# Optimization experiments

Hardware: AMD Instinct MI355X
Metric: run time of the kernel (lower is better)

Reference implementation:

```python
import jax, jax.numpy as jnp
import numpy as np

B, S, D = 2, 2048, 2048
H, HD, M = 16, 128, 8192
EPS = 1e-6

def _rmsnorm(x, scale):
    var = jnp.mean(jnp.square(x), axis=-1, keepdims=True)
    return x * jax.lax.rsqrt(var + EPS) * scale

def setup_inputs() -> dict:
    key = jax.random.key(0)
    ks = jax.random.split(key, 8)
    def init(k, shape, fan_in):
        return (jax.random.normal(k, shape, dtype=jnp.float32) / np.sqrt(fan_in)).astype(jnp.float32)
    return {
        "x": jax.random.normal(ks[0], (B, S, D), dtype=jnp.float32),
        "w_qkv": init(ks[1], (D, 3 * H * HD), D),
        "w_o": init(ks[2], (H * HD, D), H * HD),
        "w_gate": init(ks[3], (D, M), D),
        "w_up": init(ks[4], (D, M), D),
        "w_down": init(ks[5], (M, D), M),
        "rms1_scale": jnp.ones((D,), dtype=jnp.float32),
        "rms2_scale": jnp.ones((D,), dtype=jnp.float32),
    }

def reference(x, w_qkv, w_o, w_gate, w_up, w_down, rms1_scale, rms2_scale):
    batch, seq_len, embed_dim = x.shape
    # --- attention sub-block ---
    residual = x
    h = _rmsnorm(x, rms1_scale)
    qkv = h @ w_qkv  # [B,S,3*H*HD]
    qkv = qkv.reshape(batch, seq_len, 3, H, HD)
    q, k, v = qkv[:, :, 0], qkv[:, :, 1], qkv[:, :, 2]
    scale = 1.0 / jnp.sqrt(jnp.float32(HD))
    scores = jnp.einsum('bqhd,bkhd->bhqk', q, k) * scale  # materialized [B,H,S,S]
    mask = jnp.tril(jnp.ones((seq_len, seq_len), dtype=jnp.bool_))[None, None]
    scores = jnp.where(mask, scores, jnp.finfo(scores.dtype).min)
    weights = jax.nn.softmax(scores.astype(jnp.float32), axis=-1).astype(scores.dtype)
    attn_out = jnp.einsum('bhqk,bkhd->bqhd', weights, v)
    attn_out = attn_out.reshape(batch, seq_len, -1) @ w_o
    x = residual + attn_out
    # --- SwiGLU MLP sub-block ---
    residual = x
    h = _rmsnorm(x, rms2_scale)
    gate = h @ w_gate
    up = h @ w_up
    mlp = (jax.nn.silu(gate) * up) @ w_down
    return residual + mlp
```

## Files before the change

### kernel.cpp

```cpp
#include <hip/hip_runtime.h>
#include <cstdint>

#define DEV __device__ __forceinline__

typedef __attribute__((ext_vector_type(8))) short bf16x8;
typedef __attribute__((ext_vector_type(4))) float f32x4;

DEV unsigned short f2bf(float f) {
    unsigned u = __float_as_uint(f);
    return (unsigned short)((u + 0x8000u) >> 16);
}
DEV float bf2f(unsigned short h) { return __uint_as_float(((unsigned)h) << 16); }

DEV void gld_lds16(const void* g, void* l) {
    __builtin_amdgcn_global_load_lds(
        (const __attribute__((address_space(1))) unsigned int*)g,
        (__attribute__((address_space(3))) unsigned int*)l,
        16, 0, 0);
}

DEV bf16x8 scale_frag(bf16x8 v, float s) {
    bf16x8 r;
#pragma unroll
    for (int i = 0; i < 8; ++i)
        r[i] = (short)f2bf(bf2f((unsigned short)v[i]) * s);
    return r;
}

__global__ __launch_bounds__(256) void rmsnorm_kernel(const float* __restrict__ x,
                                                      const float* __restrict__ scale,
                                                      unsigned short* __restrict__ h) {
    const long row = blockIdx.x;
    const int t = threadIdx.x;
    const float4* xr = (const float4*)(x + row * 2048);
    float4 a = xr[t];
    float4 b = xr[t + 256];
    float ss = a.x*a.x + a.y*a.y + a.z*a.z + a.w*a.w
             + b.x*b.x + b.y*b.y + b.z*b.z + b.w*b.w;
#pragma unroll
    for (int off = 32; off >= 1; off >>= 1) ss += __shfl_xor(ss, off);
    __shared__ float red[4];
    if ((t & 63) == 0) red[t >> 6] = ss;
    __syncthreads();
    const float rr = rsqrtf((red[0] + red[1] + red[2] + red[3]) * (1.0f / 2048.0f) + 1e-6f);
    const float4* sc = (const float4*)scale;
    float4 s0 = sc[t], s1 = sc[t + 256];
    ushort4 o0 = make_ushort4(f2bf(a.x*rr*s0.x), f2bf(a.y*rr*s0.y), f2bf(a.z*rr*s0.z), f2bf(a.w*rr*s0.w));
    ushort4 o1 = make_ushort4(f2bf(b.x*rr*s1.x), f2bf(b.y*rr*s1.y), f2bf(b.z*rr*s1.z), f2bf(b.w*rr*s1.w));
    ushort4* hr = (ushort4*)(h + row * 2048);
    hr[t] = o0;
    hr[t + 256] = o1;
}

__global__ __launch_bounds__(256) void wcvt_kernel(const float* __restrict__ in,
                                                   unsigned short* __restrict__ out,
                                                   int K, int N) {
    __shared__ float tile[64][65];
    const int k0 = blockIdx.y * 64, n0 = blockIdx.x * 64;
    const int t = threadIdx.x;
    const int tr = t >> 4;
    const int tc = (t & 15) * 4;
#pragma unroll
    for (int p = 0; p < 4; ++p) {
        const int k = p * 16 + tr;
        float4 v = *(const float4*)&in[(long)(k0 + k) * N + n0 + tc];
        tile[k][tc] = v.x; tile[k][tc + 1] = v.y; tile[k][tc + 2] = v.z; tile[k][tc + 3] = v.w;
    }
    __syncthreads();
#pragma unroll
    for (int p = 0; p < 4; ++p) {
        const int n = p * 16 + tr;
        ushort4 o = make_ushort4(f2bf(tile[tc][n]), f2bf(tile[tc + 1][n]),
                                 f2bf(tile[tc + 2][n]), f2bf(tile[tc + 3][n]));
        *(ushort4*)&out[(long)(n0 + n) * K + k0 + tc] = o;
    }
}

template <int EPI>
__global__ __launch_bounds__(256) void gemm_kernel(const unsigned short* __restrict__ A,
                                                   const unsigned short* __restrict__ BT,
                                                   void* __restrict__ Cv,
                                                   const float* __restrict__ res,
                                                   int M, int N, int K) {
    __shared__ short A_lds[128 * 64];
    __shared__ short B_lds[128 * 64];

    const int t = threadIdx.x;
    const int wave = t >> 6, lane = t & 63;
    const int quad = lane >> 4, l16 = lane & 15;
    const int wm = wave >> 1, wn = wave & 1;
    const long m0 = (long)blockIdx.y * 128;
    const long n0 = (long)blockIdx.x * 128;

    f32x4 acc[4][4] = {};

    const int srow = lane >> 3;
    const int scol = (((lane & 7) ^ srow) << 3);

    for (int k0 = 0; k0 < K; k0 += 64) {
#pragma unroll
        for (int j = 0; j < 4; ++j) {
            gld_lds16(A + (m0 + wave * 32 + j * 8 + srow) * (long)K + k0 + scol,
                      &A_lds[(wave * 32 + j * 8) * 64]);
            gld_lds16(BT + (n0 + wave * 32 + j * 8 + srow) * (long)K + k0 + scol,
                      &B_lds[(wave * 32 + j * 8) * 64]);
        }
        __syncthreads();
#pragma unroll
        for (int ks = 0; ks < 2; ++ks) {
            bf16x8 af[4], bf[4];
#pragma unroll
            for (int i = 0; i < 4; ++i) {
                const int cs = ((ks * 4 + quad) ^ (l16 & 7)) << 3;
                af[i] = *(const bf16x8*)&A_lds[(wm * 64 + i * 16 + l16) * 64 + cs];
                bf[i] = *(const bf16x8*)&B_lds[(wn * 64 + i * 16 + l16) * 64 + cs];
            }
#pragma unroll
            for (int mt = 0; mt < 4; ++mt)
#pragma unroll
                for (int nt = 0; nt < 4; ++nt)
                    acc[mt][nt] = __builtin_amdgcn_mfma_f32_16x16x32_bf16(af[mt], bf[nt], acc[mt][nt], 0, 0, 0);
        }
        __syncthreads();
    }

#pragma unroll
    for (int mt = 0; mt < 4; ++mt) {
        const long rbase = m0 + wm * 64 + mt * 16 + quad * 4;
#pragma unroll
        for (int nt = 0; nt < 4; ++nt) {
            const long col = n0 + wn * 64 + nt * 16 + l16;
#pragma unroll
            for (int r = 0; r < 4; ++r) {
                const long idx = (rbase + r) * (long)N + col;
                const float v = acc[mt][nt][r];
                if (EPI == 0) {
                    ((unsigned short*)Cv)[idx] = f2bf(v);
                } else if (EPI == 1) {
                    ((float*)Cv)[idx] = res[idx] + v;
                } else {
                    unsigned short* C = (unsigned short*)Cv;
                    const float g = bf2f(C[idx]);
                    const float sg = g / (1.0f + __expf(-g));
                    C[idx] = f2bf(sg * v);
                }
            }
        }
    }
}

__global__ __launch_bounds__(256, 4) void attn_kernel(const unsigned short* __restrict__ qkv,
                                                      unsigned short* __restrict__ outp) {
    __shared__ short K_lds[64 * 128];
    __shared__ short V_lds[128 * 64];
    __shared__ short P_lds[4 * 16 * 64];

    const int b = blockIdx.z;
    const int qt = (b == 0) ? blockIdx.x : (31 - blockIdx.x);
    const int hh = blockIdx.y;
    const int t = threadIdx.x;
    const int wave = t >> 6, lane = t & 63, quad = lane >> 4, l16 = lane & 15;
    const long rb = (long)b * 2048;
    const int q0w = qt * 64 + wave * 16;
    const int qmax = q0w + 15;
    const float scale = 0.08838834764831845f;

    bf16x8 qf[4];
#pragma unroll
    for (int ks = 0; ks < 4; ++ks)
        qf[ks] = scale_frag(
            *(const bf16x8*)&qkv[(rb + q0w + l16) * 6144 + hh * 128 + ks * 32 + quad * 8],
            scale);

    f32x4 acc[8] = {};
    float l_lane = 0.f;

    const int ktiles = qt + 1;
    const int nc = t & 31, kq0 = (t >> 5) << 1;

    for (int kt = 0; kt < ktiles; ++kt) {
        const int k0 = kt * 64;
#pragma unroll
        for (int j = 0; j < 4; ++j) {
            const int r8 = (j * 4 + quad) & 7;
            const int csrc = ((l16 & 8) | ((l16 & 7) ^ r8)) << 3;
            gld_lds16(&qkv[(rb + k0 + wave * 16 + j * 4 + quad) * 6144 + 2048 + hh * 128 + csrc],
                      &K_lds[(wave * 16 + j * 4) * 128]);
        }
#pragma unroll
        for (int g2 = 0; g2 < 2; ++g2) {
            const int kq = kq0 + g2;
            const unsigned short* Vp = &qkv[(rb + k0 + kq * 4) * 6144 + 4096 + hh * 128 + nc * 4];
            ushort4 v0 = *(const ushort4*)Vp;
            ushort4 v1 = *(const ushort4*)(Vp + 6144);
            ushort4 v2 = *(const ushort4*)(Vp + 12288);
            ushort4 v3 = *(const ushort4*)(Vp + 18432);
            const int cs = (((kq >> 1) ^ (nc & 7)) << 3) + ((kq & 1) << 2);
            const int db = (nc * 4) * 64 + cs;
            *(ushort4*)&V_lds[db      ] = make_ushort4(v0.x, v1.x, v2.x, v3.x);
            *(ushort4*)&V_lds[db + 64 ] = make_ushort4(v0.y, v1.y, v2.y, v3.y);
            *(ushort4*)&V_lds[db + 128] = make_ushort4(v0.z, v1.z, v2.z, v3.z);
            *(ushort4*)&V_lds[db + 192] = make_ushort4(v0.w, v1.w, v2.w, v3.w);
        }
        __syncthreads();

        if (k0 <= qmax) {
            f32x4 sa[4] = {};
#pragma unroll
            for (int ks = 0; ks < 4; ++ks) {
#pragma unroll
                for (int mt = 0; mt < 4; ++mt) {
                    const int cl = ks * 4 + quad;
                    const int cphys = (cl & 8) | ((cl & 7) ^ (l16 & 7));
                    bf16x8 kf = *(const bf16x8*)&K_lds[(mt * 16 + l16) * 128 + (cphys << 3)];
                    sa[mt] = __builtin_amdgcn_mfma_f32_16x16x32_bf16(kf, qf[ks], sa[mt], 0, 0, 0);
                }
            }
            const bool domask = (k0 + 63 > q0w);
            const int qpos = q0w + l16;
#pragma unroll
            for (int mt = 0; mt < 4; ++mt) {
                const int kb = k0 + mt * 16 + quad * 4;
                ushort4 pk;
#pragma unroll
                for (int r = 0; r < 4; ++r) {
                    float s = (domask && (kb + r > qpos)) ? -1e30f : sa[mt][r];
                    float p = __expf(s);
                    l_lane += p;
                    ((unsigned short*)&pk)[r] = f2bf(p);
                }
                const int chks = (mt * 2 + (quad >> 1)) ^ (l16 & 7);
                *(ushort4*)&P_lds[wave * 1024 + l16 * 64 + chks * 8 + (quad & 1) * 4] = pk;
            }
            __asm__ __volatile__("s_waitcnt lgkmcnt(0)" ::: "memory");
#pragma unroll
            for (int kp = 0; kp < 2; ++kp) {
                bf16x8 pf = *(const bf16x8*)&P_lds[wave * 1024 + l16 * 64 +
                                                   (((kp * 4 + quad) ^ (l16 & 7)) << 3)];
#pragma unroll
                for (int dt = 0; dt < 8; ++dt) {
                    bf16x8 vf = *(const bf16x8*)&V_lds[(dt * 16 + l16) * 64 +
                                                       (((kp * 4 + quad) ^ ((dt * 4 + (l16 >> 2)) & 7)) << 3)];
                    acc[dt] = __builtin_amdgcn_mfma_f32_16x16x32_bf16(vf, pf, acc[dt], 0, 0, 0);
                }
            }
        }
        __syncthreads();
    }

    l_lane += __shfl_xor(l_lane, 16);
    l_lane += __shfl_xor(l_lane, 32);
    const float inv = 1.0f / l_lane;

    const long obase = (rb + q0w + l16) * 2048 + hh * 128;
#pragma unroll
    for (int dt = 0; dt < 8; ++dt) {
        ushort4 o;
#pragma unroll
        for (int r = 0; r < 4; ++r) ((unsigned short*)&o)[r] = f2bf(acc[dt][r] * inv);
        *(ushort4*)&outp[obase + dt * 16 + quad * 4] = o;
    }
}

extern "C" void kernel_launch(void* const* d_in, const int* in_sizes, int n_in,
                              void* d_out, int out_size, void* d_ws, size_t ws_size,
                              hipStream_t stream) {
    const float* x      = (const float*)d_in[0];
    const float* w_qkv  = (const float*)d_in[1];
    const float* w_o    = (const float*)d_in[2];
    const float* w_gate = (const float*)d_in[3];
    const float* w_up   = (const float*)d_in[4];
    const float* w_down = (const float*)d_in[5];
    const float* rms1   = (const float*)d_in[6];
    const float* rms2   = (const float*)d_in[7];
    float* out = (float*)d_out;

    char* ws = (char*)d_ws;
    unsigned short* wT      = (unsigned short*)(ws);
    unsigned short* h       = (unsigned short*)(ws + 33554432);
    unsigned short* qkv     = (unsigned short*)(ws + 50331648);
    unsigned short* attnout = (unsigned short*)(ws + 100663296);
    unsigned short* act     = qkv;

    rmsnorm_kernel<<<4096, 256, 0, stream>>>(x, rms1, h);

    wcvt_kernel<<<dim3(96, 32), 256, 0, stream>>>(w_qkv, wT, 2048, 6144);
    gemm_kernel<0><<<dim3(48, 32), 256, 0, stream>>>(h, wT, (void*)qkv, nullptr, 4096, 6144, 2048);

    attn_kernel<<<dim3(32, 16, 2), 256, 0, stream>>>(qkv, attnout);

    wcvt_kernel<<<dim3(32, 32), 256, 0, stream>>>(w_o, wT, 2048, 2048);
    gemm_kernel<1><<<dim3(16, 32), 256, 0, stream>>>(attnout, wT, (void*)out, x, 4096, 2048, 2048);

    rmsnorm_kernel<<<4096, 256, 0, stream>>>(out, rms2, h);

    wcvt_kernel<<<dim3(128, 32), 256, 0, stream>>>(w_gate, wT, 2048, 8192);
    gemm_kernel<0><<<dim3(64, 32), 256, 0, stream>>>(h, wT, (void*)act, nullptr, 4096, 8192, 2048);

    wcvt_kernel<<<dim3(128, 32), 256, 0, stream>>>(w_up, wT, 2048, 8192);
    gemm_kernel<2><<<dim3(64, 32), 256, 0, stream>>>(h, wT, (void*)act, nullptr, 4096, 8192, 2048);

    wcvt_kernel<<<dim3(32, 128), 256, 0, stream>>>(w_down, wT, 8192, 2048);
    gemm_kernel<1><<<dim3(16, 32), 256, 0, stream>>>(act, wT, (void*)out, out, 4096, 2048, 8192);
}
```

Measured before the change: 1.032 ms.

## Rewrite GEMM with larger 256xBN tiles, 8 waves, and double-buffered LDS prefetch

```diff
diff --git a/kernel.cpp b/kernel.cpp
--- a/kernel.cpp
+++ b/kernel.cpp
@@ -76,57 +76,145 @@
     }
 }
 
-template <int EPI>
-__global__ __launch_bounds__(256) void gemm_kernel(const unsigned short* __restrict__ A,
-                                                   const unsigned short* __restrict__ BT,
-                                                   void* __restrict__ Cv,
-                                                   const float* __restrict__ res,
-                                                   int M, int N, int K) {
-    __shared__ short A_lds[128 * 64];
-    __shared__ short B_lds[128 * 64];
+template <int BN, int EPI>
+__global__ __launch_bounds__(512, 2) void gemm_kernel(const unsigned short* __restrict__ A,
+                                                      const unsigned short* __restrict__ BT,
+                                                      void* __restrict__ Cv,
+                                                      const float* __restrict__ res,
+                                                      int M, int N, int K) {
+    constexpr int WN = BN / 64;
+    constexpr int WM = 8 / WN;
+    constexpr int RW = 256 / WM;
+    constexpr int MT = RW / 16;
+    constexpr int MH = MT / 2;
+
+    __shared__ short A_lds[2][256 * 64];
+    __shared__ short B_lds[2][BN * 64];
 
     const int t = threadIdx.x;
     const int wave = t >> 6, lane = t & 63;
     const int quad = lane >> 4, l16 = lane & 15;
-    const int wm = wave >> 1, wn = wave & 1;
-    const long m0 = (long)blockIdx.y * 128;
-    const long n0 = (long)blockIdx.x * 128;
-
-    f32x4 acc[4][4] = {};
+    const int wm = wave / WN, wn = wave % WN;
+    const long m0 = (long)blockIdx.y * 256;
+    const long n0 = (long)blockIdx.x * BN;
 
     const int srow = lane >> 3;
-    const int scol = (((lane & 7) ^ srow) << 3);
-
-    for (int k0 = 0; k0 < K; k0 += 64) {
-#pragma unroll
-        for (int j = 0; j < 4; ++j) {
-            gld_lds16(A + (m0 + wave * 32 + j * 8 + srow) * (long)K + k0 + scol,
-                      &A_lds[(wave * 32 + j * 8) * 64]);
-            gld_lds16(BT + (n0 + wave * 32 + j * 8 + srow) * (long)K + k0 + scol,
-                      &B_lds[(wave * 32 + j * 8) * 64]);
-        }
-        __syncthreads();
-#pragma unroll
-        for (int ks = 0; ks < 2; ++ks) {
-            bf16x8 af[4], bf[4];
-#pragma unroll
-            for (int i = 0; i < 4; ++i) {
-                const int cs = ((ks * 4 + quad) ^ (l16 & 7)) << 3;
-                af[i] = *(const bf16x8*)&A_lds[(wm * 64 + i * 16 + l16) * 64 + cs];
-                bf[i] = *(const bf16x8*)&B_lds[(wn * 64 + i * 16 + l16) * 64 + cs];
-            }
-#pragma unroll
-            for (int mt = 0; mt < 4; ++mt)
-#pragma unroll
-                for (int nt = 0; nt < 4; ++nt)
-                    acc[mt][nt] = __builtin_amdgcn_mfma_f32_16x16x32_bf16(af[mt], bf[nt], acc[mt][nt], 0, 0, 0);
-        }
-        __syncthreads();
-    }
-
-#pragma unroll
-    for (int mt = 0; mt < 4; ++mt) {
-        const long rbase = m0 + wm * 64 + mt * 16 + quad * 4;
+    const int scol = ((lane & 7) ^ srow) << 3;
+    const int nkt = K >> 6;
+
+    int aoff[MT][2], boff[4][2];
+#pragma unroll
+    for (int mt = 0; mt < MT; ++mt)
+#pragma unroll
+        for (int ks = 0; ks < 2; ++ks)
+            aoff[mt][ks] = (wm * RW + mt * 16 + l16) * 64 + ((((ks << 2) + quad) ^ (l16 & 7)) << 3);
+#pragma unroll
+    for (int nt = 0; nt < 4; ++nt)
+#pragma unroll
+        for (int ks = 0; ks < 2; ++ks)
+            boff[nt][ks] = (wn * 64 + nt * 16 + l16) * 64 + ((((ks << 2) + quad) ^ (l16 & 7)) << 3);
+
+    const unsigned short* Ag = A + (m0 + wave * 32 + srow) * (long)K + scol;
+    const unsigned short* Bg = BT + (n0 + wave * (8 * WN) + srow) * (long)K + scol;
+
+    auto stage = [&](int kt, int buf) {
+        const long kk = (long)kt << 6;
+#pragma unroll
+        for (int j = 0; j < 4; ++j)
+            gld_lds16(Ag + (long)j * 8 * K + kk, &A_lds[buf][(wave * 32 + j * 8) * 64]);
+#pragma unroll
+        for (int j = 0; j < WN; ++j)
+            gld_lds16(Bg + (long)j * 8 * K + kk, &B_lds[buf][(wave * 8 * WN + j * 8) * 64]);
+    };
+
+    f32x4 acc[MT][4] = {};
+
+    stage(0, 0);
+    stage(1, 1);
+    if constexpr (WN == 4) asm volatile("s_waitcnt vmcnt(8)" ::: "memory");
+    else                   asm volatile("s_waitcnt vmcnt(6)" ::: "memory");
+    __builtin_amdgcn_s_barrier();
+
+    int c = 0;
+    for (int kt = 0; kt < nkt; ++kt) {
+        const short* Ab = A_lds[c];
+        const short* Bb = B_lds[c];
+        bf16x8 bfr[4][2], afr[MH][2];
+#pragma unroll
+        for (int nt = 0; nt < 4; ++nt)
+#pragma unroll
+            for (int ks = 0; ks < 2; ++ks)
+                bfr[nt][ks] = *(const bf16x8*)&Bb[boff[nt][ks]];
+#pragma unroll
+        for (int mt = 0; mt < MH; ++mt)
+#pragma unroll
+            for (int ks = 0; ks < 2; ++ks)
+                afr[mt][ks] = *(const bf16x8*)&Ab[aoff[mt][ks]];
+
+        __builtin_amdgcn_s_setprio(1);
+#pragma unroll
+        for (int ks = 0; ks < 2; ++ks)
+#pragma unroll
+            for (int mt = 0; mt < MH; ++mt)
+#pragma unroll
+                for (int nt = 0; nt < 2; ++nt)
+                    acc[mt][nt] = __builtin_amdgcn_mfma_f32_16x16x32_bf16(afr[mt][ks], bfr[nt][ks], acc[mt][nt], 0, 0, 0);
+        __builtin_amdgcn_s_setprio(0);
+        __builtin_amdgcn_s_barrier();
+
+        __builtin_amdgcn_s_setprio(1);
+#pragma unroll
+        for (int ks = 0; ks < 2; ++ks)
+#pragma unroll
+            for (int mt = 0; mt < MH; ++mt)
+#pragma unroll
+                for (int nt = 2; nt < 4; ++nt)
+                    acc[mt][nt] = __builtin_amdgcn_mfma_f32_16x16x32_bf16(afr[mt][ks], bfr[nt][ks], acc[mt][nt], 0, 0, 0);
+        __builtin_amdgcn_s_setprio(0);
+        __builtin_amdgcn_s_barrier();
+
+#pragma unroll
+        for (int mt = 0; mt < MH; ++mt)
+#pragma unroll
+            for (int ks = 0; ks < 2; ++ks)
+                afr[mt][ks] = *(const bf16x8*)&Ab[aoff[MH + mt][ks]];
+        __builtin_amdgcn_s_setprio(1);
+#pragma unroll
+        for (int ks = 0; ks < 2; ++ks)
+#pragma unroll
+            for (int mt = 0; mt < MH; ++mt)
+#pragma unroll
+                for (int nt = 2; nt < 4; ++nt)
+                    acc[MH + mt][nt] = __builtin_amdgcn_mfma_f32_16x16x32_bf16(afr[mt][ks], bfr[nt][ks], acc[MH + mt][nt], 0, 0, 0);
+        __builtin_amdgcn_s_setprio(0);
+        __builtin_amdgcn_s_barrier();
+
+        __builtin_amdgcn_s_setprio(1);
+#pragma unroll
+        for (int ks = 0; ks < 2; ++ks)
+#pragma unroll
+            for (int mt = 0; mt < MH; ++mt)
+#pragma unroll
+                for (int nt = 0; nt < 2; ++nt)
+                    acc[MH + mt][nt] = __builtin_amdgcn_mfma_f32_16x16x32_bf16(afr[mt][ks], bfr[nt][ks], acc[MH + mt][nt], 0, 0, 0);
+        __builtin_amdgcn_s_setprio(0);
+
+        asm volatile("s_waitcnt lgkmcnt(0)" ::: "memory");
+        __builtin_amdgcn_s_barrier();
+        if (kt + 2 < nkt) {
+            stage(kt + 2, c);
+            if constexpr (WN == 4) asm volatile("s_waitcnt vmcnt(8)" ::: "memory");
+            else                   asm volatile("s_waitcnt vmcnt(6)" ::: "memory");
+        } else {
+            asm volatile("s_waitcnt vmcnt(0)" ::: "memory");
+        }
+        __builtin_amdgcn_s_barrier();
+        c ^= 1;
+    }
+
+#pragma unroll
+    for (int mt = 0; mt < MT; ++mt) {
+        const long rbase = m0 + wm * RW + mt * 16 + quad * 4;
 #pragma unroll
         for (int nt = 0; nt < 4; ++nt) {
             const long col = n0 + wn * 64 + nt * 16 + l16;
@@ -134,9 +222,9 @@
             for (int r = 0; r < 4; ++r) {
                 const long idx = (rbase + r) * (long)N + col;
                 const float v = acc[mt][nt][r];
-                if (EPI == 0) {
+                if constexpr (EPI == 0) {
                     ((unsigned short*)Cv)[idx] = f2bf(v);
-                } else if (EPI == 1) {
+                } else if constexpr (EPI == 1) {
                     ((float*)Cv)[idx] = res[idx] + v;
                 } else {
                     unsigned short* C = (unsigned short*)Cv;
@@ -285,21 +373,21 @@
     rmsnorm_kernel<<<4096, 256, 0, stream>>>(x, rms1, h);
 
     wcvt_kernel<<<dim3(96, 32), 256, 0, stream>>>(w_qkv, wT, 2048, 6144);
-    gemm_kernel<0><<<dim3(48, 32), 256, 0, stream>>>(h, wT, (void*)qkv, nullptr, 4096, 6144, 2048);
+    gemm_kernel<128, 0><<<dim3(48, 16), 512, 0, stream>>>(h, wT, (void*)qkv, nullptr, 4096, 6144, 2048);
 
     attn_kernel<<<dim3(32, 16, 2), 256, 0, stream>>>(qkv, attnout);
 
     wcvt_kernel<<<dim3(32, 32), 256, 0, stream>>>(w_o, wT, 2048, 2048);
-    gemm_kernel<1><<<dim3(16, 32), 256, 0, stream>>>(attnout, wT, (void*)out, x, 4096, 2048, 2048);
+    gemm_kernel<128, 1><<<dim3(16, 16), 512, 0, stream>>>(attnout, wT, (void*)out, x, 4096, 2048, 2048);
 
     rmsnorm_kernel<<<4096, 256, 0, stream>>>(out, rms2, h);
 
     wcvt_kernel<<<dim3(128, 32), 256, 0, stream>>>(w_gate, wT, 2048, 8192);
-    gemm_kernel<0><<<dim3(64, 32), 256, 0, stream>>>(h, wT, (void*)act, nullptr, 4096, 8192, 2048);
+    gemm_kernel<256, 0><<<dim3(32, 16), 512, 0, stream>>>(h, wT, (void*)act, nullptr, 4096, 8192, 2048);
 
     wcvt_kernel<<<dim3(128, 32), 256, 0, stream>>>(w_up, wT, 2048, 8192);
-    gemm_kernel<2><<<dim3(64, 32), 256, 0, stream>>>(h, wT, (void*)act, nullptr, 4096, 8192, 2048);
+    gemm_kernel<256, 2><<<dim3(32, 16), 512, 0, stream>>>(h, wT, (void*)act, nullptr, 4096, 8192, 2048);
 
     wcvt_kernel<<<dim3(32, 128), 256, 0, stream>>>(w_down, wT, 8192, 2048);
-    gemm_kernel<1><<<dim3(16, 32), 256, 0, stream>>>(act, wT, (void*)out, out, 4096, 2048, 8192);
-}
+    gemm_kernel<128, 1><<<dim3(16, 16), 512, 0, stream>>>(act, wT, (void*)out, out, 4096, 2048, 8192);
+}
```

Result: slower. 1.096 ms (+6.1%).

## Rewrite GEMM as 8-wave double-buffered pipelined kernel with larger tiles

Applied to the files above, without the earlier changes.

```diff
diff --git a/kernel.cpp b/kernel.cpp
--- a/kernel.cpp
+++ b/kernel.cpp
@@ -76,67 +76,146 @@
     }
 }
 
-template <int EPI>
-__global__ __launch_bounds__(256) void gemm_kernel(const unsigned short* __restrict__ A,
-                                                   const unsigned short* __restrict__ BT,
-                                                   void* __restrict__ Cv,
-                                                   const float* __restrict__ res,
-                                                   int M, int N, int K) {
-    __shared__ short A_lds[128 * 64];
-    __shared__ short B_lds[128 * 64];
+#define BARRIER() asm volatile("s_barrier" ::: "memory")
+#define PRE_MM()  { BARRIER(); asm volatile("s_waitcnt lgkmcnt(0)" ::: "memory"); \
+                    __builtin_amdgcn_sched_barrier(0); }
+
+#define RD_A(Ab, Mh_)                                                             \
+  { _Pragma("unroll") for (int mt = 0; mt < MTQ; ++mt)                            \
+      _Pragma("unroll") for (int ks = 0; ks < 2; ++ks)                            \
+        ar[mt][ks] = *(const bf16x8*)&(Ab)[((Mh_) * (BM / 2) + qm * (BM / 4)      \
+            + mt * 16 + l16) * 64 + ((((ks << 2) + quad) ^ axor) << 3)]; }
+
+#define RD_B(Bb, Nh_)                                                             \
+  { _Pragma("unroll") for (int nt = 0; nt < 2; ++nt)                              \
+      _Pragma("unroll") for (int ks = 0; ks < 2; ++ks)                            \
+        br[nt][ks] = *(const bf16x8*)&(Bb)[((Nh_) * 128 + qn * 32 + nt * 16       \
+            + l16) * 64 + ((((ks << 2) + quad) ^ axor) << 3)]; }
+
+#define MM(Mh_, Nh_)                                                              \
+  { __builtin_amdgcn_s_setprio(1);                                               \
+    _Pragma("unroll") for (int ks = 0; ks < 2; ++ks)                              \
+      _Pragma("unroll") for (int mt = 0; mt < MTQ; ++mt)                          \
+        _Pragma("unroll") for (int nt = 0; nt < 2; ++nt)                          \
+          acc[Mh_][mt][Nh_][nt] = __builtin_amdgcn_mfma_f32_16x16x32_bf16(        \
+              ar[mt][ks], br[nt][ks], acc[Mh_][mt][Nh_][nt], 0, 0, 0);            \
+    __builtin_amdgcn_s_setprio(0); }
+
+template <int BM, int EPI>
+__global__ __launch_bounds__(512, 2) void gemm_kernel(const unsigned short* __restrict__ A,
+                                                      const unsigned short* __restrict__ BT,
+                                                      void* __restrict__ Cv,
+                                                      const float* __restrict__ res,
+                                                      int M, int N, int K) {
+    constexpr int MTQ = BM / 64;
+    constexpr int AL  = BM / 128;
+    constexpr int VMN = 2 + AL;
+
+    __shared__ short A_lds[2][BM * 64];
+    __shared__ short B_lds[2][256 * 64];
 
     const int t = threadIdx.x;
     const int wave = t >> 6, lane = t & 63;
     const int quad = lane >> 4, l16 = lane & 15;
-    const int wm = wave >> 1, wn = wave & 1;
-    const long m0 = (long)blockIdx.y * 128;
-    const long n0 = (long)blockIdx.x * 128;
-
-    f32x4 acc[4][4] = {};
+    const int qm = wave >> 2, qn = wave & 3;
+    const long m0 = (long)blockIdx.y * BM;
+    const long n0 = (long)blockIdx.x * 256;
 
     const int srow = lane >> 3;
-    const int scol = (((lane & 7) ^ srow) << 3);
-
-    for (int k0 = 0; k0 < K; k0 += 64) {
-#pragma unroll
-        for (int j = 0; j < 4; ++j) {
-            gld_lds16(A + (m0 + wave * 32 + j * 8 + srow) * (long)K + k0 + scol,
-                      &A_lds[(wave * 32 + j * 8) * 64]);
-            gld_lds16(BT + (n0 + wave * 32 + j * 8 + srow) * (long)K + k0 + scol,
-                      &B_lds[(wave * 32 + j * 8) * 64]);
-        }
-        __syncthreads();
-#pragma unroll
-        for (int ks = 0; ks < 2; ++ks) {
-            bf16x8 af[4], bf[4];
-#pragma unroll
-            for (int i = 0; i < 4; ++i) {
-                const int cs = ((ks * 4 + quad) ^ (l16 & 7)) << 3;
-                af[i] = *(const bf16x8*)&A_lds[(wm * 64 + i * 16 + l16) * 64 + cs];
-                bf[i] = *(const bf16x8*)&B_lds[(wn * 64 + i * 16 + l16) * 64 + cs];
-            }
-#pragma unroll
-            for (int mt = 0; mt < 4; ++mt)
-#pragma unroll
-                for (int nt = 0; nt < 4; ++nt)
-                    acc[mt][nt] = __builtin_amdgcn_mfma_f32_16x16x32_bf16(af[mt], bf[nt], acc[mt][nt], 0, 0, 0);
-        }
-        __syncthreads();
-    }
-
-#pragma unroll
-    for (int mt = 0; mt < 4; ++mt) {
-        const long rbase = m0 + wm * 64 + mt * 16 + quad * 4;
-#pragma unroll
-        for (int nt = 0; nt < 4; ++nt) {
-            const long col = n0 + wn * 64 + nt * 16 + l16;
+    const int scol = ((lane & 7) ^ srow) << 3;
+    const int axor = l16 & 7;
+    const int nkt = K >> 6;
+
+    const unsigned short* Ag = A + (m0 + wave * 8 + srow) * (long)K + scol;
+    const unsigned short* Bg = BT + (n0 + wave * 8 + srow) * (long)K + scol;
+
+    auto stageA = [&](int kt, int Mh) {
+        short* dst = &A_lds[kt & 1][(Mh * (BM / 2) + wave * 8) * 64];
+        const unsigned short* src = Ag + (long)(Mh * (BM / 2)) * K + ((long)kt << 6);
+#pragma unroll
+        for (int j = 0; j < AL; ++j)
+            gld_lds16(src + (long)j * 64 * K, dst + j * 64 * 64);
+    };
+    auto stageB = [&](int kt, int Nh) {
+        short* dst = &B_lds[kt & 1][(Nh * 128 + wave * 8) * 64];
+        const unsigned short* src = Bg + (long)(Nh * 128) * K + ((long)kt << 6);
+#pragma unroll
+        for (int j = 0; j < 2; ++j)
+            gld_lds16(src + (long)j * 64 * K, dst + j * 64 * 64);
+    };
+
+    f32x4 acc[2][MTQ][2][2] = {};
+    bf16x8 ar[MTQ][2], br[2][2];
+
+    stageA(0, 0); stageA(0, 1); stageB(0, 0); stageB(0, 1);
+    stageB(1, 0); stageA(1, 1);
+    asm volatile("s_waitcnt vmcnt(%0)" :: "n"(VMN) : "memory");
+    BARRIER();
+
+    const short* A0b = A_lds[0];
+    const short* B0b = B_lds[0];
+    const short* A1b = A_lds[1];
+    const short* B1b = B_lds[1];
+
+    for (int kt = 0; kt < nkt; kt += 2) {
+        const bool more = (kt + 2) < nkt;
+
+        RD_A(A0b, 0); RD_B(B0b, 0);
+        stageB(kt + 1, 1);
+        PRE_MM(); MM(0, 0); BARRIER();
+
+        RD_A(A0b, 1);
+        stageA(kt + 1, 0);
+        PRE_MM(); MM(1, 0); BARRIER();
+
+        RD_B(B0b, 1);
+        if (more) stageB(kt + 2, 0);
+        PRE_MM(); MM(1, 1); BARRIER();
+
+        RD_A(A0b, 0);
+        if (more) stageA(kt + 2, 1);
+        PRE_MM(); MM(0, 1);
+        if (more) asm volatile("s_waitcnt vmcnt(%0)" :: "n"(VMN) : "memory");
+        else      asm volatile("s_waitcnt vmcnt(0)" ::: "memory");
+        BARRIER();
+
+        RD_A(A1b, 0); RD_B(B1b, 0);
+        if (more) stageB(kt + 2, 1);
+        PRE_MM(); MM(0, 0); BARRIER();
+
+        RD_A(A1b, 1);
+        if (more) stageA(kt + 2, 0);
+        PRE_MM(); MM(1, 0); BARRIER();
+
+        RD_B(B1b, 1);
+        if (more) stageB(kt + 3, 0);
+        PRE_MM(); MM(1, 1); BARRIER();
+
+        RD_A(A1b, 0);
+        if (more) stageA(kt + 3, 1);
+        PRE_MM(); MM(0, 1);
+        if (more) asm volatile("s_waitcnt vmcnt(%0)" :: "n"(VMN) : "memory");
+        else      asm volatile("s_waitcnt vmcnt(0)" ::: "memory");
+        BARRIER();
+    }
+
+#pragma unroll
+    for (int Mh = 0; Mh < 2; ++Mh)
+#pragma unroll
+    for (int mt = 0; mt < MTQ; ++mt) {
+        const long rbase = m0 + Mh * (BM / 2) + qm * (BM / 4) + mt * 16 + quad * 4;
+#pragma unroll
+        for (int Nh = 0; Nh < 2; ++Nh)
+#pragma unroll
+        for (int nt = 0; nt < 2; ++nt) {
+            const long col = n0 + Nh * 128 + qn * 32 + nt * 16 + l16;
 #pragma unroll
             for (int r = 0; r < 4; ++r) {
                 const long idx = (rbase + r) * (long)N + col;
-                const float v = acc[mt][nt][r];
-                if (EPI == 0) {
+                const float v = acc[Mh][mt][Nh][nt][r];
+                if constexpr (EPI == 0) {
                     ((unsigned short*)Cv)[idx] = f2bf(v);
-                } else if (EPI == 1) {
+                } else if constexpr (EPI == 1) {
                     ((float*)Cv)[idx] = res[idx] + v;
                 } else {
                     unsigned short* C = (unsigned short*)Cv;
@@ -148,6 +227,12 @@
         }
     }
 }
+
+#undef RD_A
+#undef RD_B
+#undef MM
+#undef PRE_MM
+#undef BARRIER
 
 __global__ __launch_bounds__(256, 4) void attn_kernel(const unsigned short* __restrict__ qkv,
                                                       unsigned short* __restrict__ outp) {
@@ -285,21 +370,21 @@
     rmsnorm_kernel<<<4096, 256, 0, stream>>>(x, rms1, h);
 
     wcvt_kernel<<<dim3(96, 32), 256, 0, stream>>>(w_qkv, wT, 2048, 6144);
-    gemm_kernel<0><<<dim3(48, 32), 256, 0, stream>>>(h, wT, (void*)qkv, nullptr, 4096, 6144, 2048);
+    gemm_kernel<128, 0><<<dim3(24, 32), 512, 0, stream>>>(h, wT, (void*)qkv, nullptr, 4096, 6144, 2048);
 
     attn_kernel<<<dim3(32, 16, 2), 256, 0, stream>>>(qkv, attnout);
 
     wcvt_kernel<<<dim3(32, 32), 256, 0, stream>>>(w_o, wT, 2048, 2048);
-    gemm_kernel<1><<<dim3(16, 32), 256, 0, stream>>>(attnout, wT, (void*)out, x, 4096, 2048, 2048);
+    gemm_kernel<128, 1><<<dim3(8, 32), 512, 0, stream>>>(attnout, wT, (void*)out, x, 4096, 2048, 2048);
 
     rmsnorm_kernel<<<4096, 256, 0, stream>>>(out, rms2, h);
 
     wcvt_kernel<<<dim3(128, 32), 256, 0, stream>>>(w_gate, wT, 2048, 8192);
-    gemm_kernel<0><<<dim3(64, 32), 256, 0, stream>>>(h, wT, (void*)act, nullptr, 4096, 8192, 2048);
+    gemm_kernel<256, 0><<<dim3(32, 16), 512, 0, stream>>>(h, wT, (void*)act, nullptr, 4096, 8192, 2048);
 
     wcvt_kernel<<<dim3(128, 32), 256, 0, stream>>>(w_up, wT, 2048, 8192);
-    gemm_kernel<2><<<dim3(64, 32), 256, 0, stream>>>(h, wT, (void*)act, nullptr, 4096, 8192, 2048);
+    gemm_kernel<256, 2><<<dim3(32, 16), 512, 0, stream>>>(h, wT, (void*)act, nullptr, 4096, 8192, 2048);
 
     wcvt_kernel<<<dim3(32, 128), 256, 0, stream>>>(w_down, wT, 8192, 2048);
-    gemm_kernel<1><<<dim3(16, 32), 256, 0, stream>>>(act, wT, (void*)out, out, 4096, 2048, 8192);
-}
+    gemm_kernel<128, 1><<<dim3(8, 32), 512, 0, stream>>>(act, wT, (void*)out, out, 4096, 2048, 8192);
+}
```

Measured after the change: 1.057 ms. 1.02x slower.

## Fuse gate and up GEMMs into one kernel with SiLU epilogue

Applied to the files above, without the earlier changes.

```diff
diff --git a/kernel.cpp b/kernel.cpp
--- a/kernel.cpp
+++ b/kernel.cpp
@@ -143,6 +143,88 @@
                     const float g = bf2f(C[idx]);
                     const float sg = g / (1.0f + __expf(-g));
                     C[idx] = f2bf(sg * v);
+                }
+            }
+        }
+    }
+}
+
+__global__ __launch_bounds__(512) void gemm_gateup_kernel(const unsigned short* __restrict__ A,
+                                                          const unsigned short* __restrict__ BTg,
+                                                          const unsigned short* __restrict__ BTu,
+                                                          unsigned short* __restrict__ act,
+                                                          int M, int N, int K) {
+    __shared__ short lds[3 * 128 * 64];
+    short* A_lds  = lds;
+    short* Bg_lds = lds + 8192;
+    short* Bu_lds = lds + 16384;
+
+    const int t = threadIdx.x;
+    const int wave = t >> 6, lane = t & 63;
+    const int quad = lane >> 4, l16 = lane & 15;
+    const int half = wave >> 2, w4 = wave & 3;
+    const int wm = w4 >> 1, wn = w4 & 1;
+    const long m0 = (long)blockIdx.y * 128;
+    const long n0 = (long)blockIdx.x * 128;
+
+    f32x4 acc[4][4] = {};
+
+    const int srow = lane >> 3;
+    const int scol = (((lane & 7) ^ srow) << 3);
+    const short* Bsel = half ? Bu_lds : Bg_lds;
+
+    for (int k0 = 0; k0 < K; k0 += 64) {
+#pragma unroll
+        for (int j = 0; j < 2; ++j) {
+            const int r = wave * 16 + j * 8;
+            gld_lds16(A   + (m0 + r + srow) * (long)K + k0 + scol, &A_lds[r * 64]);
+            gld_lds16(BTg + (n0 + r + srow) * (long)K + k0 + scol, &Bg_lds[r * 64]);
+            gld_lds16(BTu + (n0 + r + srow) * (long)K + k0 + scol, &Bu_lds[r * 64]);
+        }
+        __syncthreads();
+#pragma unroll
+        for (int ks = 0; ks < 2; ++ks) {
+            bf16x8 af[4], bf[4];
+#pragma unroll
+            for (int i = 0; i < 4; ++i) {
+                const int cs = ((ks * 4 + quad) ^ (l16 & 7)) << 3;
+                af[i] = *(const bf16x8*)&A_lds[(wm * 64 + i * 16 + l16) * 64 + cs];
+                bf[i] = *(const bf16x8*)&Bsel[(wn * 64 + i * 16 + l16) * 64 + cs];
+            }
+#pragma unroll
+            for (int mt = 0; mt < 4; ++mt)
+#pragma unroll
+                for (int nt = 0; nt < 4; ++nt)
+                    acc[mt][nt] = __builtin_amdgcn_mfma_f32_16x16x32_bf16(af[mt], bf[nt], acc[mt][nt], 0, 0, 0);
+        }
+        __syncthreads();
+    }
+
+    short* G = lds;
+    if (half == 0) {
+#pragma unroll
+        for (int mt = 0; mt < 4; ++mt)
+#pragma unroll
+            for (int nt = 0; nt < 4; ++nt)
+#pragma unroll
+                for (int r = 0; r < 4; ++r)
+                    G[w4 * 4096 + (mt * 16 + quad * 4 + r) * 64 + nt * 16 + l16] =
+                        (short)f2bf(acc[mt][nt][r]);
+    }
+    __syncthreads();
+    if (half == 1) {
+#pragma unroll
+        for (int mt = 0; mt < 4; ++mt) {
+            const long rbase = m0 + wm * 64 + mt * 16 + quad * 4;
+#pragma unroll
+            for (int nt = 0; nt < 4; ++nt) {
+                const long col = n0 + wn * 64 + nt * 16 + l16;
+#pragma unroll
+                for (int r = 0; r < 4; ++r) {
+                    const float g = bf2f((unsigned short)
+                        G[w4 * 4096 + (mt * 16 + quad * 4 + r) * 64 + nt * 16 + l16]);
+                    const float sg = g / (1.0f + __expf(-g));
+                    act[(rbase + r) * (long)N + col] = f2bf(sg * acc[mt][nt][r]);
                 }
             }
         }
@@ -206,6 +288,7 @@
 
         if (k0 <= qmax) {
             f32x4 sa[4] = {};
+            __builtin_amdgcn_s_setprio(1);
 #pragma unroll
             for (int ks = 0; ks < 4; ++ks) {
 #pragma unroll
@@ -216,6 +299,7 @@
                     sa[mt] = __builtin_amdgcn_mfma_f32_16x16x32_bf16(kf, qf[ks], sa[mt], 0, 0, 0);
                 }
             }
+            __builtin_amdgcn_s_setprio(0);
             const bool domask = (k0 + 63 > q0w);
             const int qpos = q0w + l16;
 #pragma unroll
@@ -233,6 +317,7 @@
                 *(ushort4*)&P_lds[wave * 1024 + l16 * 64 + chks * 8 + (quad & 1) * 4] = pk;
             }
             __asm__ __volatile__("s_waitcnt lgkmcnt(0)" ::: "memory");
+            __builtin_amdgcn_s_setprio(1);
 #pragma unroll
             for (int kp = 0; kp < 2; ++kp) {
                 bf16x8 pf = *(const bf16x8*)&P_lds[wave * 1024 + l16 * 64 +
@@ -244,6 +329,7 @@
                     acc[dt] = __builtin_amdgcn_mfma_f32_16x16x32_bf16(vf, pf, acc[dt], 0, 0, 0);
                 }
             }
+            __builtin_amdgcn_s_setprio(0);
         }
         __syncthreads();
     }
@@ -281,6 +367,7 @@
     unsigned short* qkv     = (unsigned short*)(ws + 50331648);
     unsigned short* attnout = (unsigned short*)(ws + 100663296);
     unsigned short* act     = qkv;
+    unsigned short* wTu     = (unsigned short*)(ws + 117440512);
 
     rmsnorm_kernel<<<4096, 256, 0, stream>>>(x, rms1, h);
 
@@ -294,11 +381,16 @@
 
     rmsnorm_kernel<<<4096, 256, 0, stream>>>(out, rms2, h);
 
-    wcvt_kernel<<<dim3(128, 32), 256, 0, stream>>>(w_gate, wT, 2048, 8192);
-    gemm_kernel<0><<<dim3(64, 32), 256, 0, stream>>>(h, wT, (void*)act, nullptr, 4096, 8192, 2048);
-
-    wcvt_kernel<<<dim3(128, 32), 256, 0, stream>>>(w_up, wT, 2048, 8192);
-    gemm_kernel<2><<<dim3(64, 32), 256, 0, stream>>>(h, wT, (void*)act, nullptr, 4096, 8192, 2048);
+    if (ws_size >= 150994944) {
+        wcvt_kernel<<<dim3(128, 32), 256, 0, stream>>>(w_gate, wT, 2048, 8192);
+        wcvt_kernel<<<dim3(128, 32), 256, 0, stream>>>(w_up, wTu, 2048, 8192);
+        gemm_gateup_kernel<<<dim3(64, 32), 512, 0, stream>>>(h, wT, wTu, act, 4096, 8192, 2048);
+    } else {
+        wcvt_kernel<<<dim3(128, 32), 256, 0, stream>>>(w_gate, wT, 2048, 8192);
+        gemm_kernel<0><<<dim3(64, 32), 256, 0, stream>>>(h, wT, (void*)act, nullptr, 4096, 8192, 2048);
+        wcvt_kernel<<<dim3(128, 32), 256, 0, stream>>>(w_up, wT, 2048, 8192);
+        gemm_kernel<2><<<dim3(64, 32), 256, 0, stream>>>(h, wT, (void*)act, nullptr, 4096, 8192, 2048);
+    }
 
     wcvt_kernel<<<dim3(32, 128), 256, 0, stream>>>(w_down, wT, 8192, 2048);
     gemm_kernel<1><<<dim3(16, 32), 256, 0, stream>>>(act, wT, (void*)out, out, 4096, 2048, 8192);
```

After: 972.0 us. 1.06x faster.
